# Performance work log

Measured on AMD Instinct MI355X. Metric: run time of the kernel, lower is better.

Reference implementation:

```python
import jax, jax.numpy as jnp
import numpy as np

B, S, D, H, HD = 8, 1374, 384, 6, 64
NUM_PATCHES = 1369  # (518 // 14) ** 2
NUM_PREFIX = 5      # 1 cls + 4 registers


def setup_inputs() -> dict:
    key = jax.random.key(0)
    ks = jax.random.split(key, 10)
    init = 0.02  # truncated_normal(0.02) approximated by scaled normal
    x = jax.random.normal(ks[0], (B, S, D), jnp.float32)
    wq = jax.random.truncated_normal(ks[1], -2.0, 2.0, (D, H, HD), jnp.float32) * init
    wk = jax.random.truncated_normal(ks[2], -2.0, 2.0, (D, H, HD), jnp.float32) * init
    wv = jax.random.truncated_normal(ks[3], -2.0, 2.0, (D, H, HD), jnp.float32) * init
    wo = jax.random.truncated_normal(ks[4], -2.0, 2.0, (H, HD, D), jnp.float32) * init
    bq = jnp.zeros((H, HD), jnp.float32)
    bk = jnp.zeros((H, HD), jnp.float32)
    bv = jnp.zeros((H, HD), jnp.float32)
    bo = jnp.zeros((D,), jnp.float32)
    keep_patch_indices = jax.random.randint(ks[5], (B, NUM_PATCHES), 0, NUM_PATCHES).astype(jnp.int64)
    return {"x": x, "wq": wq, "bq": bq, "wk": wk, "bk": bk, "wv": wv, "bv": bv,
            "wo": wo, "bo": bo, "keep_patch_indices": keep_patch_indices, "k_patches": 685}


def reference(x, wq, bq, wk, bk, wv, bv, wo, bo, keep_patch_indices, k_patches):
    # q/k/v projections: DenseGeneral to (heads, head_dim)
    q = jnp.einsum('bsd,dhe->bshe', x, wq) + bq
    k = jnp.einsum('bsd,dhe->bshe', x, wk) + bk
    v = jnp.einsum('bsd,dhe->bshe', x, wv) + bv

    z = jnp.einsum('bqhd,bkhd->bhqk', q / (HD ** 0.5), k)  # [B,H,S,S]
    attn_logits = z  # saved BEFORE masking (used by 'mse' criterion)

    # dynamic scatter mask: patch columns >= k_patches get -inf
    num_selected = keep_patch_indices.shape[1]
    patch_idx = jnp.arange(num_selected)
    indices_to_mask = jnp.where(patch_idx >= k_patches, patch_idx, num_selected) + NUM_PREFIX
    # out-of-bounds indices (== num_selected + NUM_PREFIX) are dropped by JAX scatter semantics
    z = z.at[:, :, :, indices_to_mask].set(-jnp.inf)

    attn_map = jax.nn.softmax(z, axis=-1)
    zo = jnp.einsum('bhqk,bkhd->bqhd', attn_map, v)
    output = jnp.einsum('bqhd,hdo->bqo', zo, wo) + bo  # wo contracts (heads, head_dim)

    # attn_aggregate = ['cls_token','reg_token','patch_token'], zoom_map_criterion='mse'
    am = attn_logits.mean(axis=1)  # mean over heads -> [B,S,S]
    aggs = jnp.stack([
        am[:, 0:1, :].mean(axis=1),      # cls token
        am[:, 1:5, :].mean(axis=1),      # register tokens
        am[:, 5:1374, :].mean(axis=1),   # patch tokens
    ], axis=1)                            # [B,3,S]
    attn_agg = aggs.mean(axis=1)          # [B,S]
    return output, attn_agg
```

## Files before the change

### kernel.cpp

```cpp
#include <hip/hip_runtime.h>
#include <stdint.h>

#define BB 8
#define SS 1374
#define DD 384
#define HH 6
#define HDIM 64
#define MROWS (BB*SS)
#define NPFX 5
#define SPAD 1376

typedef __attribute__((ext_vector_type(8))) short bf16x8;
typedef __attribute__((ext_vector_type(4))) float f32x4;
typedef __attribute__((ext_vector_type(2))) unsigned int u32x2;
typedef __attribute__((ext_vector_type(4))) unsigned int u32x4;
typedef u32x4 __attribute__((aligned(4))) u32x4_u;

__device__ __forceinline__ unsigned short f2bf(float f){
  union { float f; unsigned int u; } v; v.f = f;
  return (unsigned short)((v.u + 0x7FFFu + ((v.u >> 16) & 1u)) >> 16);
}
__device__ __forceinline__ float bf2f(unsigned short b){
  union { float f; unsigned int u; } v; v.u = ((unsigned int)b) << 16; return v.f;
}
__device__ __forceinline__ unsigned int pk_bf16(float a, float b){
#if __has_builtin(__builtin_amdgcn_cvt_pk_bf16_f32)
  typedef __attribute__((ext_vector_type(2))) __bf16 bfv2;
  bfv2 p = __builtin_amdgcn_cvt_pk_bf16_f32(a, b);
  union { bfv2 v; unsigned int u; } c; c.v = p; return c.u;
#else
  return (unsigned int)f2bf(a) | ((unsigned int)f2bf(b) << 16);
#endif
}

__global__ void k_prep_x(const float* __restrict__ x, unsigned short* __restrict__ xb,
                         float* __restrict__ xbar){
  int b = blockIdx.x / 43, ch = blockIdx.x % 43;
  int d = threadIdx.x;
  int s0 = ch*32, s1 = s0 + 32; if (s1 > SS) s1 = SS;
  float acc = 0.f;
  for (int s = s0; s < s1; ++s){
    float v = x[((size_t)b*SS + s)*DD + d];
    float w = (s == 0) ? (1.f/3.f) : (s < 5) ? (1.f/12.f) : (1.f/4107.f);
    acc += w * v;
    xb[((size_t)b*SS + s)*DD + d] = f2bf(v);
  }
  atomicAdd(&xbar[b*DD + d], acc);
}

__global__ void k_conv_w(const float* __restrict__ wq, const float* __restrict__ wk,
                         const float* __restrict__ wv, const float* __restrict__ wo,
                         unsigned short* __restrict__ wbT, unsigned short* __restrict__ woT){
  int i = blockIdx.x*blockDim.x + threadIdx.x;
  if (i < 1152*384){
    int n = i / 384, d = i % 384;
    const float* w = (n < 384) ? wq : (n < 768) ? wk : wv;
    wbT[i] = f2bf(w[(size_t)d*384 + (n % 384)]);
  } else if (i < 1152*384 + 384*384){
    int j = i - 1152*384;
    int n = j / 384, k = j % 384;
    woT[j] = f2bf(wo[(size_t)k*384 + n]);
  }
}

__global__ void k_qbar(const float* __restrict__ xbar, const float* __restrict__ wq,
                       const float* __restrict__ bq, float* __restrict__ qbar){
  __shared__ float xs[DD];
  int b = blockIdx.x, t = threadIdx.x;
  xs[t] = xbar[b*DD + t];
  __syncthreads();
  float acc = bq[t];
  for (int d = 0; d < DD; ++d) acc += xs[d]*wq[(size_t)d*384 + t];
  qbar[b*384 + t] = acc;
}

__global__ void k_agg(const float* __restrict__ qbar, const unsigned short* __restrict__ kg,
                      float* __restrict__ out_agg){
  __shared__ float qs[384];
  int b = blockIdx.x / 6, sb = blockIdx.x % 6;
  int t = threadIdx.x;
  for (int i = t; i < 384; i += 256) qs[i] = qbar[b*384 + i];
  __syncthreads();
  int s = sb*256 + t;
  if (s >= SS) return;
  float acc = 0.f;
  for (int h = 0; h < HH; ++h){
    const unsigned short* kr = kg + (((size_t)(b*HH + h))*SS + s)*64;
    const float* qh = qs + h*64;
    for (int c = 0; c < 8; ++c){
      u32x4 v = *(const u32x4*)(kr + c*8);
      #pragma unroll
      for (int j = 0; j < 4; ++j){
        unsigned int u = v[j];
        acc += qh[c*8 + 2*j]     * bf2f((unsigned short)(u & 0xFFFFu));
        acc += qh[c*8 + 2*j + 1] * bf2f((unsigned short)(u >> 16));
      }
    }
  }
  out_agg[b*SS + s] = acc * (1.f/48.f);
}

template<int MODE>
__global__ __launch_bounds__(256) void k_gemm(
    const unsigned short* __restrict__ A, const unsigned short* __restrict__ Bt,
    const float* __restrict__ b0, const float* __restrict__ b1, const float* __restrict__ b2,
    unsigned short* __restrict__ qg, unsigned short* __restrict__ kgp,
    unsigned short* __restrict__ vt, float* __restrict__ out,
    const int* __restrict__ kpat)
{
  int mt = blockIdx.x % 86, nt = blockIdx.x / 86;
  const int t = threadIdx.x;
  const int w = t >> 6, lane = t & 63, quad = lane >> 4, l16 = lane & 15;
  const int wm = w >> 1, wn = w & 1;
  const int m0 = mt*128, n0 = nt*64;

  if (MODE == 0 && nt >= 12){
    int s0r_ = m0 % SS;
    int SKv = NPFX + kpat[0]; if (SKv > SS) SKv = SS; if (SKv < 1) SKv = 1;
    int lo = (SKv + 63) & ~63;
    if (s0r_ >= lo && s0r_ + 127 < SS) return;
  }

  constexpr int SMEM_SH = (MODE==0) ? 13824 : 17408;
  __shared__ unsigned short smem[SMEM_SH];
  unsigned short* As = smem;
  unsigned short* Bs = smem + 9216;
  f32x4 acc[4][2];
  #pragma unroll
  for (int i=0;i<4;i++){ acc[i][0] = (f32x4){0,0,0,0}; acc[i][1] = (f32x4){0,0,0,0}; }

  const int ar = t >> 1, akb = (t & 1) * 32;
  int ga = m0 + ar; if (ga > MROWS-1) ga = MROWS-1;
  const unsigned short* ap = A + (size_t)ga*384 + akb;
  const int br = t >> 2, bkb = (t & 3) * 16;
  const unsigned short* bp = Bt + (size_t)(n0 + br)*384 + bkb;

  u32x4 ra[4], rb[2];
  #pragma unroll
  for (int i=0;i<4;i++) ra[i] = *(const u32x4*)(ap + i*8);
  rb[0] = *(const u32x4*)(bp); rb[1] = *(const u32x4*)(bp + 8);

  for (int kc = 0; kc < 6; ++kc){
    __syncthreads();
    #pragma unroll
    for (int i=0;i<4;i++) *(u32x4*)(As + ar*72 + akb + i*8) = ra[i];
    *(u32x4*)(Bs + br*72 + bkb)     = rb[0];
    *(u32x4*)(Bs + br*72 + bkb + 8) = rb[1];
    __syncthreads();
    if (kc + 1 < 6){
      int kn = (kc+1)*64;
      #pragma unroll
      for (int i=0;i<4;i++) ra[i] = *(const u32x4*)(ap + kn + i*8);
      rb[0] = *(const u32x4*)(bp + kn); rb[1] = *(const u32x4*)(bp + kn + 8);
    }
    #pragma unroll
    for (int kh = 0; kh < 2; ++kh){
      bf16x8 af[4], bfr[2];
      #pragma unroll
      for (int rf = 0; rf < 4; ++rf)
        af[rf] = *(const bf16x8*)(As + (wm*64 + rf*16 + l16)*72 + kh*32 + quad*8);
      #pragma unroll
      for (int cf = 0; cf < 2; ++cf)
        bfr[cf] = *(const bf16x8*)(Bs + (wn*32 + cf*16 + l16)*72 + kh*32 + quad*8);
      #pragma unroll
      for (int rf = 0; rf < 4; ++rf)
        #pragma unroll
        for (int cf = 0; cf < 2; ++cf)
          acc[rf][cf] = __builtin_amdgcn_mfma_f32_16x16x32_bf16(af[rf], bfr[cf], acc[rf][cf], 0,0,0);
    }
  }

  const int b0r = m0 / SS, s0r = m0 % SS;
  __syncthreads();
  if (MODE == 1){
    float* CsF = (float*)smem;
    #pragma unroll
    for (int cf = 0; cf < 2; ++cf){
      int e = wn*32 + cf*16 + l16;
      float bias = b0[n0 + e];
      #pragma unroll
      for (int rf = 0; rf < 4; ++rf){
        int rr = wm*64 + rf*16 + quad*4;
        #pragma unroll
        for (int r4 = 0; r4 < 4; ++r4)
          CsF[(rr + r4)*68 + e] = acc[rf][cf][r4] + bias;
      }
    }
    __syncthreads();
    #pragma unroll
    for (int p = 0; p < 8; ++p){
      int r = p*16 + (t >> 4), c = t & 15;
      int rr = m0 + r;
      if (rr < MROWS){
        f32x4 v = *(const f32x4*)(CsF + r*68 + c*4);
        *(f32x4*)(out + (size_t)rr*384 + n0 + c*4) = v;
      }
    }
  } else {
    const int mat = nt / 6, h = nt - mat*6;
    const float* bvp = (mat==0) ? b0 : (mat==1) ? b1 : b2;
    const float vsc = (mat==0) ? 0.125f : 1.f;
    if (mat < 2){
      unsigned short* Cs = As;
      unsigned short* dst = (mat==0) ? qg : kgp;
      #pragma unroll
      for (int cf = 0; cf < 2; ++cf){
        int e = wn*32 + cf*16 + l16;
        float bias = bvp[h*64 + e];
        #pragma unroll
        for (int rf = 0; rf < 4; ++rf){
          int rr = wm*64 + rf*16 + quad*4;
          #pragma unroll
          for (int r4 = 0; r4 < 4; ++r4)
            Cs[(rr + r4)*72 + e] = f2bf((acc[rf][cf][r4] + bias)*vsc);
        }
      }
      __syncthreads();
      #pragma unroll
      for (int p = 0; p < 4; ++p){
        int r = p*32 + (t >> 3), c = t & 7;
        int rr = m0 + r;
        if (rr < MROWS){
          int s = s0r + r, bb = b0r;
          if (s >= SS){ s -= SS; ++bb; }
          u32x4 v = *(const u32x4*)(Cs + r*72 + c*8);
          *(u32x4*)(dst + (((size_t)(bb*HH + h))*SS + s)*64 + c*8) = v;
        }
      }
    } else {
      unsigned short* CsV = As;
      #pragma unroll
      for (int cf = 0; cf < 2; ++cf){
        int e = wn*32 + cf*16 + l16;
        float bias = bvp[h*64 + e];
        #pragma unroll
        for (int rf = 0; rf < 4; ++rf){
          int rr = wm*64 + rf*16 + quad*4;
          #pragma unroll
          for (int p = 0; p < 2; ++p)
            *(unsigned int*)(CsV + e*136 + rr + p*2) =
                pk_bf16(acc[rf][cf][p*2] + bias, acc[rf][cf][p*2+1] + bias);
        }
      }
      __syncthreads();
      const bool nowrap = (s0r + 127 < SS) && (m0 + 127 < MROWS);
      if (nowrap){
        int e = t >> 2;
        unsigned short* vrow = vt + ((size_t)(b0r*HH + h)*64 + e)*SPAD + s0r;
        #pragma unroll
        for (int i = 0; i < 4; ++i){
          int c = (t & 3)*4 + i;
          u32x4 v = *(const u32x4*)(CsV + e*136 + c*8);
          *(u32x4_u*)(vrow + c*8) = v;
        }
      } else {
        for (int idx = t; idx < 64*64; idx += 256){
          int e = idx >> 6, sp = (idx & 63)*2;
          int rr = m0 + sp;
          if (rr < MROWS){
            int s = s0r + sp, bb = b0r;
            if (s >= SS){ s -= SS; ++bb; }
            *(unsigned int*)(vt + ((size_t)(bb*HH + h)*64 + e)*SPAD + s) =
                *(const unsigned int*)(CsV + e*136 + sp);
          }
        }
      }
    }
  }
}

#define KSTR 72
__global__ __launch_bounds__(256) void k_attn(
    const unsigned short* __restrict__ qg, const unsigned short* __restrict__ kg,
    const unsigned short* __restrict__ vt, unsigned short* __restrict__ zo,
    const int* __restrict__ kpat)
{
  const int NQB = 22;
  int qb = blockIdx.x % NQB, bh = blockIdx.x / NQB;
  int t = threadIdx.x, w = t >> 6, lane = t & 63, quad = lane >> 4, l16 = lane & 15;
  int SK = NPFX + kpat[0]; if (SK > SS) SK = SS; if (SK < 1) SK = 1;
  int niter = (SK + 63) >> 6;
  __shared__ unsigned short Ks[2][64*KSTR];
  __shared__ unsigned short Vs[2][64*KSTR];
  __shared__ unsigned short Ps[4][16*KSTR];
  unsigned short* Pw = &Ps[w][0];
  int q0 = qb*64 + w*16;

  bf16x8 aq[2];
  {
    int qrow = q0 + l16; if (qrow > SS-1) qrow = SS-1;
    const unsigned short* p = qg + ((size_t)bh*SS + qrow)*64;
    aq[0] = *(const bf16x8*)(p + quad*8);
    aq[1] = *(const bf16x8*)(p + 32 + quad*8);
  }
  f32x4 o[4];
  float rsum[4] = {0.f,0.f,0.f,0.f};
  #pragma unroll
  for (int i=0;i<4;i++) o[i] = (f32x4){0.f,0.f,0.f,0.f};

  const int srow = t >> 2, sc = (t & 3) * 16;
  const unsigned short* kbase = kg + ((size_t)bh*SS)*64;
  const unsigned short* vbase = vt + ((size_t)bh*64)*SPAD;
  u32x4 rk[2], rv[2];
  {
    int krow = srow; if (krow > SS-1) krow = SS-1;
    rk[0] = *(const u32x4*)(kbase + (size_t)krow*64 + sc);
    rk[1] = *(const u32x4*)(kbase + (size_t)krow*64 + sc + 8);
    rv[0] = *(const u32x4*)(vbase + (size_t)srow*SPAD + sc);
    rv[1] = *(const u32x4*)(vbase + (size_t)srow*SPAD + sc + 8);
  }

  for (int it = 0; it < niter; ++it){
    int k0 = it*64;
    int cur = it & 1;
    unsigned short* Ksc = &Ks[cur][0];
    unsigned short* Vsc = &Vs[cur][0];
    *(u32x4*)(Ksc + srow*KSTR + sc)     = rk[0];
    *(u32x4*)(Ksc + srow*KSTR + sc + 8) = rk[1];
    *(u32x4*)(Vsc + srow*KSTR + sc)     = rv[0];
    *(u32x4*)(Vsc + srow*KSTR + sc + 8) = rv[1];
    __syncthreads();
    if (it + 1 < niter){
      int kn = k0 + 64;
      int krow = kn + srow; if (krow > SS-1) krow = SS-1;
      rk[0] = *(const u32x4*)(kbase + (size_t)krow*64 + sc);
      rk[1] = *(const u32x4*)(kbase + (size_t)krow*64 + sc + 8);
      rv[0] = *(const u32x4*)(vbase + (size_t)srow*SPAD + kn + sc);
      rv[1] = *(const u32x4*)(vbase + (size_t)srow*SPAD + kn + sc + 8);
    }
    bool tail = (k0 + 64 > SK);
    #pragma unroll
    for (int ks = 0; ks < 2; ++ks){
      float pp[2][4];
      #pragma unroll
      for (int ns = 0; ns < 2; ++ns){
        f32x4 zf = (f32x4){0.f,0.f,0.f,0.f};
        #pragma unroll
        for (int ec = 0; ec < 2; ++ec){
          bf16x8 bkf = *(const bf16x8*)(Ksc + (ks*32 + 2*l16 + ns)*KSTR + ec*32 + quad*8);
          zf = __builtin_amdgcn_mfma_f32_16x16x32_bf16(aq[ec], bkf, zf, 0,0,0);
        }
        bool valid = !tail || (k0 + ks*32 + 2*l16 + ns) < SK;
        #pragma unroll
        for (int rg = 0; rg < 4; ++rg) pp[ns][rg] = valid ? __expf(zf[rg]) : 0.f;
      }
      #pragma unroll
      for (int rg = 0; rg < 4; ++rg){
        rsum[rg] += pp[0][rg] + pp[1][rg];
        *(unsigned int*)(Pw + (quad*4 + rg)*KSTR + ks*32 + 2*l16) =
            pk_bf16(pp[0][rg], pp[1][rg]);
      }
    }
    #pragma unroll
    for (int kc = 0; kc < 2; ++kc){
      bf16x8 ap = *(const bf16x8*)(Pw + l16*KSTR + kc*32 + quad*8);
      #pragma unroll
      for (int nc = 0; nc < 4; ++nc){
        bf16x8 vf = *(const bf16x8*)(Vsc + (nc*16 + l16)*KSTR + kc*32 + quad*8);
        o[nc] = __builtin_amdgcn_mfma_f32_16x16x32_bf16(ap, vf, o[nc], 0,0,0);
      }
    }
  }
  int b = bh / HH, h = bh - (bh/HH)*HH;
  #pragma unroll
  for (int rg = 0; rg < 4; ++rg){
    float s = rsum[rg];
    #pragma unroll
    for (int off = 8; off >= 1; off >>= 1) s += __shfl_xor(s, off);
    int q = q0 + quad*4 + rg;
    if (q >= SS) continue;
    float inv = 1.f / s;
    unsigned short* dst = zo + ((size_t)b*SS + q)*384 + h*64;
    #pragma unroll
    for (int nc = 0; nc < 4; ++nc) dst[nc*16 + l16] = f2bf(o[nc][rg]*inv);
  }
}

extern "C" void kernel_launch(void* const* d_in, const int* in_sizes, int n_in,
                              void* d_out, int out_size, void* d_ws, size_t ws_size,
                              hipStream_t stream){
  const float* x  = (const float*)d_in[0];
  const float* wq = (const float*)d_in[1];
  const float* bq = (const float*)d_in[2];
  const float* wk = (const float*)d_in[3];
  const float* bk = (const float*)d_in[4];
  const float* wv = (const float*)d_in[5];
  const float* bv = (const float*)d_in[6];
  const float* wo = (const float*)d_in[7];
  const float* bo = (const float*)d_in[8];
  const int* kpat = (const int*)d_in[10];
  float* out = (float*)d_out;
  float* out_agg = out + (size_t)MROWS*DD;

  char* ws = (char*)d_ws;
  unsigned short* xb  = (unsigned short*)(ws);
  unsigned short* wbT = (unsigned short*)(ws +  8441856);
  unsigned short* woT = (unsigned short*)(ws +  9326592);
  unsigned short* qg  = (unsigned short*)(ws +  9621504);
  unsigned short* kg  = (unsigned short*)(ws + 18063360);
  unsigned short* vt  = (unsigned short*)(ws + 26505216);
  unsigned short* zo  = (unsigned short*)(ws + 34959360);
  float* xbar         = (float*)(ws + 43401216);
  float* qbar         = (float*)(ws + 43413504);
  (void)in_sizes; (void)n_in; (void)out_size; (void)ws_size;

  hipMemsetAsync(xbar, 0, BB*DD*sizeof(float), stream);
  k_prep_x<<<BB*43, DD, 0, stream>>>(x, xb, xbar);
  k_conv_w<<<((1152*384 + 384*384) + 255)/256, 256, 0, stream>>>(wq, wk, wv, wo, wbT, woT);
  k_qbar<<<BB, DD, 0, stream>>>(xbar, wq, bq, qbar);
  k_gemm<0><<<86*18, 256, 0, stream>>>(xb, wbT, bq, bk, bv, qg, kg, vt, nullptr, kpat);
  k_attn<<<48*22, 256, 0, stream>>>(qg, kg, vt, zo, kpat);
  k_agg<<<BB*6, 256, 0, stream>>>(qbar, kg, out_agg);
  k_gemm<1><<<86*6, 256, 0, stream>>>(zo, woT, bo, nullptr, nullptr, nullptr, nullptr, nullptr, out, nullptr);
}
```

Measured before the change: 182.9 us.

## Fuse prep kernels, fold agg into K epilogue, widen attention tiles, remap XCDs

Combines the x-prep and weight-conversion kernels into one launch and removes the separate aggregation kernel by computing qbar·k dot products in the K-projection epilogue with atomics. The attention kernel now handles 32 query rows per wave (128 per block), reusing each K/V fragment across two MFMA row tiles. Block indices are remapped across XCDs for cache locality, and the LDS row stride changes to 68. Risks include misaligned 16-byte LDS reads with the new stride, more register pressure in attention, and atomic contention on the aggregation output.

```diff
diff --git a/kernel.cpp b/kernel.cpp
--- a/kernel.cpp
+++ b/kernel.cpp
@@ -12,7 +12,6 @@
 
 typedef __attribute__((ext_vector_type(8))) short bf16x8;
 typedef __attribute__((ext_vector_type(4))) float f32x4;
-typedef __attribute__((ext_vector_type(2))) unsigned int u32x2;
 typedef __attribute__((ext_vector_type(4))) unsigned int u32x4;
 typedef u32x4 __attribute__((aligned(4))) u32x4_u;
 
@@ -33,33 +32,41 @@
 #endif
 }
 
-__global__ void k_prep_x(const float* __restrict__ x, unsigned short* __restrict__ xb,
-                         float* __restrict__ xbar){
-  int b = blockIdx.x / 43, ch = blockIdx.x % 43;
-  int d = threadIdx.x;
-  int s0 = ch*32, s1 = s0 + 32; if (s1 > SS) s1 = SS;
-  float acc = 0.f;
-  for (int s = s0; s < s1; ++s){
-    float v = x[((size_t)b*SS + s)*DD + d];
-    float w = (s == 0) ? (1.f/3.f) : (s < 5) ? (1.f/12.f) : (1.f/4107.f);
-    acc += w * v;
-    xb[((size_t)b*SS + s)*DD + d] = f2bf(v);
-  }
-  atomicAdd(&xbar[b*DD + d], acc);
-}
-
-__global__ void k_conv_w(const float* __restrict__ wq, const float* __restrict__ wk,
-                         const float* __restrict__ wv, const float* __restrict__ wo,
-                         unsigned short* __restrict__ wbT, unsigned short* __restrict__ woT){
-  int i = blockIdx.x*blockDim.x + threadIdx.x;
-  if (i < 1152*384){
-    int n = i / 384, d = i % 384;
-    const float* w = (n < 384) ? wq : (n < 768) ? wk : wv;
-    wbT[i] = f2bf(w[(size_t)d*384 + (n % 384)]);
-  } else if (i < 1152*384 + 384*384){
-    int j = i - 1152*384;
-    int n = j / 384, k = j % 384;
-    woT[j] = f2bf(wo[(size_t)k*384 + n]);
+__device__ __forceinline__ int xcd_remap(int i, int n){
+  int q = n >> 3, r = n & 7;
+  int x = i & 7, j = i >> 3;
+  return (x < r ? x*(q+1) : r*(q+1) + (x - r)*q) + j;
+}
+
+__global__ void k_prep(const float* __restrict__ x, const float* __restrict__ wq,
+                       const float* __restrict__ wk, const float* __restrict__ wv,
+                       const float* __restrict__ wo,
+                       unsigned short* __restrict__ xb, float* __restrict__ xbar,
+                       unsigned short* __restrict__ wbT, unsigned short* __restrict__ woT){
+  int bid = blockIdx.x, t = threadIdx.x;
+  if (bid < BB*43){
+    int b = bid / 43, ch = bid % 43;
+    int d = t;
+    int s0 = ch*32, s1 = s0 + 32; if (s1 > SS) s1 = SS;
+    float acc = 0.f;
+    for (int s = s0; s < s1; ++s){
+      float v = x[((size_t)b*SS + s)*DD + d];
+      float w = (s == 0) ? (1.f/3.f) : (s < 5) ? (1.f/12.f) : (1.f/4107.f);
+      acc += w * v;
+      xb[((size_t)b*SS + s)*DD + d] = f2bf(v);
+    }
+    atomicAdd(&xbar[b*DD + d], acc);
+  } else {
+    int i = (bid - BB*43)*384 + t;
+    if (i < 1152*384){
+      int n = i / 384, d = i % 384;
+      const float* w = (n < 384) ? wq : (n < 768) ? wk : wv;
+      wbT[i] = f2bf(w[(size_t)d*384 + (n % 384)]);
+    } else {
+      int j = i - 1152*384;
+      int n = j / 384, k = j % 384;
+      woT[j] = f2bf(wo[(size_t)k*384 + n]);
+    }
   }
 }
 
@@ -74,41 +81,17 @@
   qbar[b*384 + t] = acc;
 }
 
-__global__ void k_agg(const float* __restrict__ qbar, const unsigned short* __restrict__ kg,
-                      float* __restrict__ out_agg){
-  __shared__ float qs[384];
-  int b = blockIdx.x / 6, sb = blockIdx.x % 6;
-  int t = threadIdx.x;
-  for (int i = t; i < 384; i += 256) qs[i] = qbar[b*384 + i];
-  __syncthreads();
-  int s = sb*256 + t;
-  if (s >= SS) return;
-  float acc = 0.f;
-  for (int h = 0; h < HH; ++h){
-    const unsigned short* kr = kg + (((size_t)(b*HH + h))*SS + s)*64;
-    const float* qh = qs + h*64;
-    for (int c = 0; c < 8; ++c){
-      u32x4 v = *(const u32x4*)(kr + c*8);
-      #pragma unroll
-      for (int j = 0; j < 4; ++j){
-        unsigned int u = v[j];
-        acc += qh[c*8 + 2*j]     * bf2f((unsigned short)(u & 0xFFFFu));
-        acc += qh[c*8 + 2*j + 1] * bf2f((unsigned short)(u >> 16));
-      }
-    }
-  }
-  out_agg[b*SS + s] = acc * (1.f/48.f);
-}
-
 template<int MODE>
 __global__ __launch_bounds__(256) void k_gemm(
     const unsigned short* __restrict__ A, const unsigned short* __restrict__ Bt,
     const float* __restrict__ b0, const float* __restrict__ b1, const float* __restrict__ b2,
     unsigned short* __restrict__ qg, unsigned short* __restrict__ kgp,
     unsigned short* __restrict__ vt, float* __restrict__ out,
-    const int* __restrict__ kpat)
+    const int* __restrict__ kpat, const float* __restrict__ qbar, float* __restrict__ oagg)
 {
-  int mt = blockIdx.x % 86, nt = blockIdx.x / 86;
+  const int NT = (MODE==0) ? 18 : 6;
+  int wg = xcd_remap(blockIdx.x, 86*NT);
+  int mt = wg / NT, nt = wg % NT;
   const int t = threadIdx.x;
   const int w = t >> 6, lane = t & 63, quad = lane >> 4, l16 = lane & 15;
   const int wm = w >> 1, wn = w & 1;
@@ -225,6 +208,20 @@
           if (s >= SS){ s -= SS; ++bb; }
           u32x4 v = *(const u32x4*)(Cs + r*72 + c*8);
           *(u32x4*)(dst + (((size_t)(bb*HH + h))*SS + s)*64 + c*8) = v;
+          if (mat == 1){
+            const float* qh = qbar + bb*384 + h*64 + c*8;
+            float part = 0.f;
+            #pragma unroll
+            for (int j = 0; j < 4; ++j){
+              unsigned int u = v[j];
+              part += qh[2*j]     * bf2f((unsigned short)(u & 0xFFFFu));
+              part += qh[2*j + 1] * bf2f((unsigned short)(u >> 16));
+            }
+            part += __shfl_xor(part, 1);
+            part += __shfl_xor(part, 2);
+            part += __shfl_xor(part, 4);
+            if (c == 0) atomicAdd(oagg + bb*SS + s, part * (1.f/48.f));
+          }
         }
       }
     } else {
@@ -269,43 +266,46 @@
   }
 }
 
-#define KSTR 72
+#define KSTR 68
 __global__ __launch_bounds__(256) void k_attn(
     const unsigned short* __restrict__ qg, const unsigned short* __restrict__ kg,
     const unsigned short* __restrict__ vt, unsigned short* __restrict__ zo,
     const int* __restrict__ kpat)
 {
-  const int NQB = 22;
-  int qb = blockIdx.x % NQB, bh = blockIdx.x / NQB;
+  const int NQB = 11;
+  int wg = xcd_remap(blockIdx.x, 48*NQB);
+  int qb = wg % NQB, bh = wg / NQB;
   int t = threadIdx.x, w = t >> 6, lane = t & 63, quad = lane >> 4, l16 = lane & 15;
   int SK = NPFX + kpat[0]; if (SK > SS) SK = SS; if (SK < 1) SK = 1;
   int niter = (SK + 63) >> 6;
   __shared__ unsigned short Ks[2][64*KSTR];
   __shared__ unsigned short Vs[2][64*KSTR];
-  __shared__ unsigned short Ps[4][16*KSTR];
+  __shared__ unsigned short Ps[4][32*KSTR];
   unsigned short* Pw = &Ps[w][0];
-  int q0 = qb*64 + w*16;
-
-  bf16x8 aq[2];
-  {
-    int qrow = q0 + l16; if (qrow > SS-1) qrow = SS-1;
+  int q0 = qb*128 + w*32;
+
+  bf16x8 aq[2][2];
+  #pragma unroll
+  for (int rt = 0; rt < 2; ++rt){
+    int qrow = q0 + rt*16 + l16; if (qrow > SS-1) qrow = SS-1;
     const unsigned short* p = qg + ((size_t)bh*SS + qrow)*64;
-    aq[0] = *(const bf16x8*)(p + quad*8);
-    aq[1] = *(const bf16x8*)(p + 32 + quad*8);
-  }
-  f32x4 o[4];
-  float rsum[4] = {0.f,0.f,0.f,0.f};
+    aq[rt][0] = *(const bf16x8*)(p + quad*8);
+    aq[rt][1] = *(const bf16x8*)(p + 32 + quad*8);
+  }
+  f32x4 o[2][4];
+  float rsum[2][4];
   #pragma unroll
-  for (int i=0;i<4;i++) o[i] = (f32x4){0.f,0.f,0.f,0.f};
+  for (int rt=0;rt<2;++rt)
+    #pragma unroll
+    for (int i=0;i<4;i++){ o[rt][i] = (f32x4){0.f,0.f,0.f,0.f}; rsum[rt][i] = 0.f; }
 
   const int srow = t >> 2, sc = (t & 3) * 16;
   const unsigned short* kbase = kg + ((size_t)bh*SS)*64;
   const unsigned short* vbase = vt + ((size_t)bh*64)*SPAD;
   u32x4 rk[2], rv[2];
   {
-    int krow = srow; if (krow > SS-1) krow = SS-1;
-    rk[0] = *(const u32x4*)(kbase + (size_t)krow*64 + sc);
-    rk[1] = *(const u32x4*)(kbase + (size_t)krow*64 + sc + 8);
+    rk[0] = *(const u32x4*)(kbase + (size_t)srow*64 + sc);
+    rk[1] = *(const u32x4*)(kbase + (size_t)srow*64 + sc + 8);
     rv[0] = *(const u32x4*)(vbase + (size_t)srow*SPAD + sc);
     rv[1] = *(const u32x4*)(vbase + (size_t)srow*SPAD + sc + 8);
   }
@@ -331,49 +331,58 @@
     bool tail = (k0 + 64 > SK);
     #pragma unroll
     for (int ks = 0; ks < 2; ++ks){
-      float pp[2][4];
-      #pragma unroll
-      for (int ns = 0; ns < 2; ++ns){
-        f32x4 zf = (f32x4){0.f,0.f,0.f,0.f};
-        #pragma unroll
-        for (int ec = 0; ec < 2; ++ec){
-          bf16x8 bkf = *(const bf16x8*)(Ksc + (ks*32 + 2*l16 + ns)*KSTR + ec*32 + quad*8);
-          zf = __builtin_amdgcn_mfma_f32_16x16x32_bf16(aq[ec], bkf, zf, 0,0,0);
-        }
-        bool valid = !tail || (k0 + ks*32 + 2*l16 + ns) < SK;
-        #pragma unroll
-        for (int rg = 0; rg < 4; ++rg) pp[ns][rg] = valid ? __expf(zf[rg]) : 0.f;
-      }
-      #pragma unroll
-      for (int rg = 0; rg < 4; ++rg){
-        rsum[rg] += pp[0][rg] + pp[1][rg];
-        *(unsigned int*)(Pw + (quad*4 + rg)*KSTR + ks*32 + 2*l16) =
-            pk_bf16(pp[0][rg], pp[1][rg]);
+      bf16x8 bkf[2][2];
+      #pragma unroll
+      for (int ns = 0; ns < 2; ++ns)
+        #pragma unroll
+        for (int ec = 0; ec < 2; ++ec)
+          bkf[ns][ec] = *(const bf16x8*)(Ksc + (ks*32 + 2*l16 + ns)*KSTR + ec*32 + quad*8);
+      bool v0 = !tail || (k0 + ks*32 + 2*l16)     < SK;
+      bool v1 = !tail || (k0 + ks*32 + 2*l16 + 1) < SK;
+      #pragma unroll
+      for (int rt = 0; rt < 2; ++rt){
+        f32x4 z0 = (f32x4){0.f,0.f,0.f,0.f};
+        f32x4 z1 = (f32x4){0.f,0.f,0.f,0.f};
+        z0 = __builtin_amdgcn_mfma_f32_16x16x32_bf16(aq[rt][0], bkf[0][0], z0, 0,0,0);
+        z0 = __builtin_amdgcn_mfma_f32_16x16x32_bf16(aq[rt][1], bkf[0][1], z0, 0,0,0);
+        z1 = __builtin_amdgcn_mfma_f32_16x16x32_bf16(aq[rt][0], bkf[1][0], z1, 0,0,0);
+        z1 = __builtin_amdgcn_mfma_f32_16x16x32_bf16(aq[rt][1], bkf[1][1], z1, 0,0,0);
+        #pragma unroll
+        for (int rg = 0; rg < 4; ++rg){
+          float p0 = v0 ? __expf(z0[rg]) : 0.f;
+          float p1 = v1 ? __expf(z1[rg]) : 0.f;
+          rsum[rt][rg] += p0 + p1;
+          *(unsigned int*)(Pw + (rt*16 + quad*4 + rg)*KSTR + ks*32 + 2*l16) = pk_bf16(p0, p1);
+        }
       }
     }
     #pragma unroll
     for (int kc = 0; kc < 2; ++kc){
-      bf16x8 ap = *(const bf16x8*)(Pw + l16*KSTR + kc*32 + quad*8);
+      bf16x8 ap0 = *(const bf16x8*)(Pw + l16*KSTR + kc*32 + quad*8);
+      bf16x8 ap1 = *(const bf16x8*)(Pw + (16 + l16)*KSTR + kc*32 + quad*8);
       #pragma unroll
       for (int nc = 0; nc < 4; ++nc){
         bf16x8 vf = *(const bf16x8*)(Vsc + (nc*16 + l16)*KSTR + kc*32 + quad*8);
-        o[nc] = __builtin_amdgcn_mfma_f32_16x16x32_bf16(ap, vf, o[nc], 0,0,0);
+        o[0][nc] = __builtin_amdgcn_mfma_f32_16x16x32_bf16(ap0, vf, o[0][nc], 0,0,0);
+        o[1][nc] = __builtin_amdgcn_mfma_f32_16x16x32_bf16(ap1, vf, o[1][nc], 0,0,0);
       }
     }
   }
   int b = bh / HH, h = bh - (bh/HH)*HH;
   #pragma unroll
-  for (int rg = 0; rg < 4; ++rg){
-    float s = rsum[rg];
-    #pragma unroll
-    for (int off = 8; off >= 1; off >>= 1) s += __shfl_xor(s, off);
-    int q = q0 + quad*4 + rg;
-    if (q >= SS) continue;
-    float inv = 1.f / s;
-    unsigned short* dst = zo + ((size_t)b*SS + q)*384 + h*64;
-    #pragma unroll
-    for (int nc = 0; nc < 4; ++nc) dst[nc*16 + l16] = f2bf(o[nc][rg]*inv);
-  }
+  for (int rt = 0; rt < 2; ++rt)
+    #pragma unroll
+    for (int rg = 0; rg < 4; ++rg){
+      float s = rsum[rt][rg];
+      #pragma unroll
+      for (int off = 8; off >= 1; off >>= 1) s += __shfl_xor(s, off);
+      int q = q0 + rt*16 + quad*4 + rg;
+      if (q >= SS) continue;
+      float inv = 1.f / s;
+      unsigned short* dst = zo + ((size_t)b*SS + q)*384 + h*64;
+      #pragma unroll
+      for (int nc = 0; nc < 4; ++nc) dst[nc*16 + l16] = f2bf(o[rt][nc][rg]*inv);
+    }
 }
 
 extern "C" void kernel_launch(void* const* d_in, const int* in_sizes, int n_in,
@@ -405,11 +414,10 @@
   (void)in_sizes; (void)n_in; (void)out_size; (void)ws_size;
 
   hipMemsetAsync(xbar, 0, BB*DD*sizeof(float), stream);
-  k_prep_x<<<BB*43, DD, 0, stream>>>(x, xb, xbar);
-  k_conv_w<<<((1152*384 + 384*384) + 255)/256, 256, 0, stream>>>(wq, wk, wv, wo, wbT, woT);
+  hipMemsetAsync(out_agg, 0, BB*SS*sizeof(float), stream);
+  k_prep<<<BB*43 + 1536, 384, 0, stream>>>(x, wq, wk, wv, wo, xb, xbar, wbT, woT);
   k_qbar<<<BB, DD, 0, stream>>>(xbar, wq, bq, qbar);
-  k_gemm<0><<<86*18, 256, 0, stream>>>(xb, wbT, bq, bk, bv, qg, kg, vt, nullptr, kpat);
-  k_attn<<<48*22, 256, 0, stream>>>(qg, kg, vt, zo, kpat);
-  k_agg<<<BB*6, 256, 0, stream>>>(qbar, kg, out_agg);
-  k_gemm<1><<<86*6, 256, 0, stream>>>(zo, woT, bo, nullptr, nullptr, nullptr, nullptr, nullptr, out, nullptr);
-}
+  k_gemm<0><<<86*18, 256, 0, stream>>>(xb, wbT, bq, bk, bv, qg, kg, vt, nullptr, kpat, qbar, out_agg);
+  k_attn<<<48*11, 256, 0, stream>>>(qg, kg, vt, zo, kpat);
+  k_gemm<1><<<86*6, 256, 0, stream>>>(zo, woT, bo, nullptr, nullptr, nullptr, nullptr, nullptr, out, nullptr, nullptr, nullptr);
+}
```

New measurement: 229.6 us. 25.5% more time.
